# Optimization experiments

Measured on AMD Instinct MI355X. Metric: run time of the kernel, lower is better.

Reference implementation:

```python
import jax, jax.numpy as jnp
import numpy as np

N = 100000
E = 1600000
IN, HID, OUT = 128, 64, 32


def setup_inputs() -> dict:
    key = jax.random.key(0)
    k1, k2, k3, k4, k5, k6 = jax.random.split(key, 6)
    x = jax.random.normal(k1, (N, IN), dtype=jnp.float32)
    edge_index = jax.random.randint(k2, (2, E), 0, N, dtype=jnp.int64)
    # Glorot-style init for the two GCNConv layers (weight + bias each)
    W1 = jax.random.normal(k3, (IN, HID), dtype=jnp.float32) / np.sqrt(IN)
    b1 = jnp.zeros((HID,), dtype=jnp.float32)
    W2 = jax.random.normal(k4, (HID, OUT), dtype=jnp.float32) / np.sqrt(HID)
    b2 = jnp.zeros((OUT,), dtype=jnp.float32)
    return {"x": x, "edge_index": edge_index, "W1": W1, "b1": b1, "W2": W2, "b2": b2}


def _gcn_norm(edge_index, n, dtype):
    """Add self-loops and compute symmetric normalization coefficients.
    Returns (row, col, norm) where norm[e] = deg[row]^-1/2 * deg[col]^-1/2."""
    loops = jnp.tile(jnp.arange(n, dtype=edge_index.dtype)[None, :], (2, 1))
    ei = jnp.concatenate([edge_index, loops], axis=1)  # [2, E+N]
    row, col = ei[0], ei[1]
    deg = jax.ops.segment_sum(jnp.ones(col.shape, dtype), col, num_segments=n)
    dinv = jnp.where(deg > 0, jax.lax.rsqrt(deg), 0.0)
    norm = dinv[row] * dinv[col]
    return row, col, norm


def _gcn_conv(h, W, b, row, col, norm, n):
    h = h @ W                                   # [N, F_out] dense transform first
    msg = h[row] * norm[:, None]                # gather + edge-normalize
    out = jax.ops.segment_sum(msg, col, num_segments=n)  # scatter-add
    return out + b


def reference(x, edge_index, W1, b1, W2, b2):
    n = x.shape[0]
    row, col, norm = _gcn_norm(edge_index, n, x.dtype)
    h = jax.nn.relu(_gcn_conv(x, W1, b1, row, col, norm, n))
    return _gcn_conv(h, W2, b2, row, col, norm, n)
```

## Files before the change

kernel.cpp:

```cpp
#include <hip/hip_runtime.h>


#define CDIV(a, b) (((a) + (b)-1) / (b))
#define EDGE_TILE 4096
#define BUCKET_CAP 4608

__device__ inline unsigned short f2bf(float f) {
    unsigned int u = __float_as_uint(f);
    u += 0x7FFF + ((u >> 16) & 1);
    return (unsigned short)(u >> 16);
}
__device__ inline void bf2x2(unsigned int u, float& lo, float& hi) {
    lo = __uint_as_float(u << 16);
    hi = __uint_as_float(u & 0xFFFF0000u);
}

__global__ __launch_bounds__(256, 4) void k_sort_gemm1(
    const int* __restrict__ row, const int* __restrict__ col, int e,
    int* __restrict__ gcur, int* __restrict__ bucket,
    const float* __restrict__ x, const float* __restrict__ W,
    unsigned short* __restrict__ hb, int n, int nb_sort) {
    __shared__ int smem[8192];
    int t = threadIdx.x;
    if ((int)blockIdx.x < nb_sort) {
        int* lstart = smem;
        int* rbase  = smem + 512;
        int* hist   = smem + 1024;
        int* ent    = smem + 1536;
        unsigned short* bid = (unsigned short*)(smem + 5632);
        int base = blockIdx.x * EDGE_TILE;
        int cnt = min(EDGE_TILE, e - base);
        hist[t] = 0; hist[t + 256] = 0;
        __syncthreads();
        for (int i = t; i < cnt; i += 256) atomicAdd(&hist[col[base + i] >> 8], 1);
        __syncthreads();
        int h0 = hist[2 * t], h1 = hist[2 * t + 1];
        int sum2 = h0 + h1;
        rbase[t] = sum2;
        __syncthreads();
        for (int d = 1; d < 256; d <<= 1) {
            int v = (t >= d) ? rbase[t - d] : 0;
            __syncthreads();
            rbase[t] += v;
            __syncthreads();
        }
        int excl2 = rbase[t] - sum2;
        __syncthreads();
        lstart[2 * t] = excl2;
        lstart[2 * t + 1] = excl2 + h0;
        for (int b = t; b < 512; b += 256) {
            int hbv = hist[b];
            rbase[b] = (hbv > 0) ? atomicAdd(&gcur[b], hbv) : 0;
            hist[b] = 0;
        }
        __syncthreads();
        for (int i = t; i < cnt; i += 256) {
            int c = col[base + i], r = row[base + i];
            int b = c >> 8;
            int rk = atomicAdd(&hist[b], 1);
            int p = lstart[b] + rk;
            ent[p] = ((c & 255) << 17) | r;
            bid[p] = (unsigned short)b;
        }
        __syncthreads();
        for (int i = t; i < cnt; i += 256) {
            int b = bid[i];
            int gi = rbase[b] + (i - lstart[b]);
            if (gi < BUCKET_CAP) bucket[(size_t)b * BUCKET_CAP + gi] = ent[i];
        }
    } else {
        float4* xs = (float4*)smem;
        int base = ((int)blockIdx.x - nb_sort) * 64;
        int nodes = min(64, n - base);
        const float4* xg = (const float4*)(x + (size_t)base * 128);
        int lim = nodes * 32;
#pragma unroll
        for (int i = 0; i < 8; ++i) {
            int idx = t + i * 256;
            if (idx < lim) xs[idx] = xg[idx];
        }
        __syncthreads();
        int j = t & 63, g = t >> 6;
        float acc[16];
#pragma unroll
        for (int mm = 0; mm < 16; ++mm) acc[mm] = 0.f;
#pragma unroll 8
        for (int k4 = 0; k4 < 32; ++k4) {
            float w0 = W[(k4 * 4 + 0) * 64 + j];
            float w1 = W[(k4 * 4 + 1) * 64 + j];
            float w2 = W[(k4 * 4 + 2) * 64 + j];
            float w3 = W[(k4 * 4 + 3) * 64 + j];
#pragma unroll
            for (int mm = 0; mm < 16; ++mm) {
                float4 xv = xs[(mm * 4 + g) * 32 + k4];
                acc[mm] = fmaf(xv.x, w0, acc[mm]);
                acc[mm] = fmaf(xv.y, w1, acc[mm]);
                acc[mm] = fmaf(xv.z, w2, acc[mm]);
                acc[mm] = fmaf(xv.w, w3, acc[mm]);
            }
        }
#pragma unroll
        for (int mm = 0; mm < 16; ++mm) {
            int m = base + mm * 4 + g;
            if (m < n) hb[(size_t)m * 64 + j] = f2bf(acc[mm]);
        }
    }
}

__global__ __launch_bounds__(256) void k_csr(
    const int* __restrict__ gcur, const int* __restrict__ bucket,
    int* __restrict__ csr, int* __restrict__ start, int* __restrict__ cntg,
    float* __restrict__ dinv, int n) {
    __shared__ int hist[256], lstart[256], lcur[256], sc[256];
    __shared__ int csrbuf[BUCKET_CAP];
    int b = blockIdx.x, t = threadIdx.x;
    int nb = gridDim.x;
    int* gball = csrbuf;
    int v0 = (2 * t < nb) ? min(gcur[2 * t], BUCKET_CAP) : 0;
    int v1 = (2 * t + 1 < nb) ? min(gcur[2 * t + 1], BUCKET_CAP) : 0;
    int s2 = v0 + v1;
    sc[t] = s2;
    __syncthreads();
    for (int d = 1; d < 256; d <<= 1) {
        int a = (t >= d) ? sc[t - d] : 0;
        __syncthreads();
        sc[t] += a;
        __syncthreads();
    }
    int excl2 = sc[t] - s2;
    gball[2 * t] = excl2;
    gball[2 * t + 1] = excl2 + v0;
    __syncthreads();
    int gb = gball[b];
    int nodebase = b << 8;
    int nnode = min(256, n - nodebase);
    int m = min(gcur[b], BUCKET_CAP);
    const int* ent = bucket + (size_t)b * BUCKET_CAP;
    __syncthreads();
    hist[t] = 0;
    __syncthreads();
    for (int i = t; i < m; i += 256) atomicAdd(&hist[ent[i] >> 17], 1);
    __syncthreads();
    int v = hist[t];
    lstart[t] = v;
    __syncthreads();
    for (int d = 1; d < 256; d <<= 1) {
        int a = (t >= d) ? lstart[t - d] : 0;
        __syncthreads();
        lstart[t] += a;
        __syncthreads();
    }
    int excl = lstart[t] - v;
    if (t < nnode) {
        int node = nodebase + t;
        start[node] = gb + excl;
        cntg[node] = v;
        dinv[node] = rsqrtf((float)(v + 1));
    }
    __syncthreads();
    lstart[t] = excl;
    lcur[t] = 0;
    __syncthreads();
    for (int i = t; i < m; i += 256) {
        int en = ent[i];
        int local = en >> 17;
        int rk = atomicAdd(&lcur[local], 1);
        csrbuf[lstart[local] + rk] = en & 0x1FFFF;
    }
    __syncthreads();
    for (int i = t; i < m; i += 256) csr[gb + i] = csrbuf[i];
}

__global__ __launch_bounds__(256) void k_agg1(const int* __restrict__ start,
                                              const int* __restrict__ cnt,
                                              const int* __restrict__ csr,
                                              const float* __restrict__ dinv,
                                              const unsigned short* __restrict__ hbm,
                                              const float* __restrict__ b,
                                              const float* __restrict__ W2,
                                              unsigned short* __restrict__ h2b, int n) {
    __shared__ float rowbuf[4][64];
    int node = (blockIdx.x * 256 + threadIdx.x) >> 6;
    int w = threadIdx.x >> 6;
    int lane = threadIdx.x & 63;
    int q = lane >> 3;
    int f4 = lane & 7;
    const int* cs = csr + start[node];
    int d = cnt[node];
    float dc = dinv[node];
    const uint4* hb = (const uint4*)hbm;
    float a0[8], a1[8];
#pragma unroll
    for (int k = 0; k < 8; ++k) { a0[k] = 0.f; a1[k] = 0.f; }
    int j = q;
    for (; j + 8 < d; j += 16) {
        int r0 = cs[j], r1 = cs[j + 8];
        float d0 = dinv[r0], d1 = dinv[r1];
        uint4 v0 = hb[(size_t)r0 * 8 + f4];
        uint4 v1 = hb[(size_t)r1 * 8 + f4];
        float lo, hi;
        bf2x2(v0.x, lo, hi); a0[0] = fmaf(lo, d0, a0[0]); a0[1] = fmaf(hi, d0, a0[1]);
        bf2x2(v0.y, lo, hi); a0[2] = fmaf(lo, d0, a0[2]); a0[3] = fmaf(hi, d0, a0[3]);
        bf2x2(v0.z, lo, hi); a0[4] = fmaf(lo, d0, a0[4]); a0[5] = fmaf(hi, d0, a0[5]);
        bf2x2(v0.w, lo, hi); a0[6] = fmaf(lo, d0, a0[6]); a0[7] = fmaf(hi, d0, a0[7]);
        bf2x2(v1.x, lo, hi); a1[0] = fmaf(lo, d1, a1[0]); a1[1] = fmaf(hi, d1, a1[1]);
        bf2x2(v1.y, lo, hi); a1[2] = fmaf(lo, d1, a1[2]); a1[3] = fmaf(hi, d1, a1[3]);
        bf2x2(v1.z, lo, hi); a1[4] = fmaf(lo, d1, a1[4]); a1[5] = fmaf(hi, d1, a1[5]);
        bf2x2(v1.w, lo, hi); a1[6] = fmaf(lo, d1, a1[6]); a1[7] = fmaf(hi, d1, a1[7]);
    }
    if (j < d) {
        int r = cs[j];
        float d0 = dinv[r];
        uint4 v0 = hb[(size_t)r * 8 + f4];
        float lo, hi;
        bf2x2(v0.x, lo, hi); a0[0] = fmaf(lo, d0, a0[0]); a0[1] = fmaf(hi, d0, a0[1]);
        bf2x2(v0.y, lo, hi); a0[2] = fmaf(lo, d0, a0[2]); a0[3] = fmaf(hi, d0, a0[3]);
        bf2x2(v0.z, lo, hi); a0[4] = fmaf(lo, d0, a0[4]); a0[5] = fmaf(hi, d0, a0[5]);
        bf2x2(v0.w, lo, hi); a0[6] = fmaf(lo, d0, a0[6]); a0[7] = fmaf(hi, d0, a0[7]);
    }
#pragma unroll
    for (int k = 0; k < 8; ++k) a0[k] += a1[k];
#pragma unroll
    for (int k = 0; k < 8; ++k) {
        a0[k] += __shfl_xor(a0[k], 8, 64);
        a0[k] += __shfl_xor(a0[k], 16, 64);
        a0[k] += __shfl_xor(a0[k], 32, 64);
    }
    if (q == 0) {
        uint4 sv = hb[(size_t)node * 8 + f4];
        float s[8], lo, hi;
        bf2x2(sv.x, lo, hi); s[0] = lo; s[1] = hi;
        bf2x2(sv.y, lo, hi); s[2] = lo; s[3] = hi;
        bf2x2(sv.z, lo, hi); s[4] = lo; s[5] = hi;
        bf2x2(sv.w, lo, hi); s[6] = lo; s[7] = hi;
        const float4* b4 = (const float4*)b;
        float4 bv0 = b4[f4 * 2], bv1 = b4[f4 * 2 + 1];
        rowbuf[w][f4 * 8 + 0] = fmaxf(fmaf(s[0], dc, a0[0]) * dc + bv0.x, 0.f);
        rowbuf[w][f4 * 8 + 1] = fmaxf(fmaf(s[1], dc, a0[1]) * dc + bv0.y, 0.f);
        rowbuf[w][f4 * 8 + 2] = fmaxf(fmaf(s[2], dc, a0[2]) * dc + bv0.z, 0.f);
        rowbuf[w][f4 * 8 + 3] = fmaxf(fmaf(s[3], dc, a0[3]) * dc + bv0.w, 0.f);
        rowbuf[w][f4 * 8 + 4] = fmaxf(fmaf(s[4], dc, a0[4]) * dc + bv1.x, 0.f);
        rowbuf[w][f4 * 8 + 5] = fmaxf(fmaf(s[5], dc, a0[5]) * dc + bv1.y, 0.f);
        rowbuf[w][f4 * 8 + 6] = fmaxf(fmaf(s[6], dc, a0[6]) * dc + bv1.z, 0.f);
        rowbuf[w][f4 * 8 + 7] = fmaxf(fmaf(s[7], dc, a0[7]) * dc + bv1.w, 0.f);
    }
    __syncthreads();
    int jj = lane & 31, half = lane >> 5;
    const float* rw = rowbuf[w] + half * 32;
    const float* Wk = W2 + half * 32 * 32 + jj;
    float acc = 0.f;
#pragma unroll 8
    for (int k = 0; k < 32; ++k) acc = fmaf(rw[k], Wk[k * 32], acc);
    acc += __shfl_xor(acc, 32, 64);
    if (half == 0) h2b[(size_t)node * 32 + jj] = f2bf(acc * dc);
}

__global__ __launch_bounds__(256) void k_agg2(const int* __restrict__ start,
                                              const int* __restrict__ cnt,
                                              const int* __restrict__ csr,
                                              const float* __restrict__ dinv,
                                              const unsigned short* __restrict__ hbm,
                                              const float* __restrict__ b,
                                              float* __restrict__ out, int n) {
    int node = (blockIdx.x * 256 + threadIdx.x) >> 6;
    if (node >= n) return;
    int lane = threadIdx.x & 63;
    int q = lane >> 2;
    int f4 = lane & 3;
    const int* cs = csr + start[node];
    int d = cnt[node];
    const uint4* hb = (const uint4*)hbm;
    float a0[8], a1[8];
#pragma unroll
    for (int k = 0; k < 8; ++k) { a0[k] = 0.f; a1[k] = 0.f; }
    int j = q;
    for (; j + 16 < d; j += 32) {
        int r0 = cs[j], r1 = cs[j + 16];
        uint4 v0 = hb[(size_t)r0 * 4 + f4];
        uint4 v1 = hb[(size_t)r1 * 4 + f4];
        float lo, hi;
        bf2x2(v0.x, lo, hi); a0[0] += lo; a0[1] += hi;
        bf2x2(v0.y, lo, hi); a0[2] += lo; a0[3] += hi;
        bf2x2(v0.z, lo, hi); a0[4] += lo; a0[5] += hi;
        bf2x2(v0.w, lo, hi); a0[6] += lo; a0[7] += hi;
        bf2x2(v1.x, lo, hi); a1[0] += lo; a1[1] += hi;
        bf2x2(v1.y, lo, hi); a1[2] += lo; a1[3] += hi;
        bf2x2(v1.z, lo, hi); a1[4] += lo; a1[5] += hi;
        bf2x2(v1.w, lo, hi); a1[6] += lo; a1[7] += hi;
    }
    if (j < d) {
        int r = cs[j];
        uint4 v0 = hb[(size_t)r * 4 + f4];
        float lo, hi;
        bf2x2(v0.x, lo, hi); a0[0] += lo; a0[1] += hi;
        bf2x2(v0.y, lo, hi); a0[2] += lo; a0[3] += hi;
        bf2x2(v0.z, lo, hi); a0[4] += lo; a0[5] += hi;
        bf2x2(v0.w, lo, hi); a0[6] += lo; a0[7] += hi;
    }
#pragma unroll
    for (int k = 0; k < 8; ++k) a0[k] += a1[k];
#pragma unroll
    for (int k = 0; k < 8; ++k) {
        a0[k] += __shfl_xor(a0[k], 4, 64);
        a0[k] += __shfl_xor(a0[k], 8, 64);
        a0[k] += __shfl_xor(a0[k], 16, 64);
        a0[k] += __shfl_xor(a0[k], 32, 64);
    }
    if (q == 0) {
        float dc = dinv[node];
        uint4 sv = hb[(size_t)node * 4 + f4];
        float s[8], lo, hi;
        bf2x2(sv.x, lo, hi); s[0] = lo; s[1] = hi;
        bf2x2(sv.y, lo, hi); s[2] = lo; s[3] = hi;
        bf2x2(sv.z, lo, hi); s[4] = lo; s[5] = hi;
        bf2x2(sv.w, lo, hi); s[6] = lo; s[7] = hi;
        const float4* b4 = (const float4*)b;
        float4 bv0 = b4[f4 * 2], bv1 = b4[f4 * 2 + 1];
        float4 o0, o1;
        o0.x = (a0[0] + s[0]) * dc + bv0.x;
        o0.y = (a0[1] + s[1]) * dc + bv0.y;
        o0.z = (a0[2] + s[2]) * dc + bv0.z;
        o0.w = (a0[3] + s[3]) * dc + bv0.w;
        o1.x = (a0[4] + s[4]) * dc + bv1.x;
        o1.y = (a0[5] + s[5]) * dc + bv1.y;
        o1.z = (a0[6] + s[6]) * dc + bv1.z;
        o1.w = (a0[7] + s[7]) * dc + bv1.w;
        float4* o4 = (float4*)out;
        o4[(size_t)node * 8 + f4 * 2]     = o0;
        o4[(size_t)node * 8 + f4 * 2 + 1] = o1;
    }
}

extern "C" void kernel_launch(void* const* d_in, const int* in_sizes, int n_in,
                              void* d_out, int out_size, void* d_ws, size_t ws_size,
                              hipStream_t stream) {
    const float* x  = (const float*)d_in[0];
    const int*   ei = (const int*)d_in[1];
    const float* W1 = (const float*)d_in[2];
    const float* b1 = (const float*)d_in[3];
    const float* W2 = (const float*)d_in[4];
    const float* b2 = (const float*)d_in[5];
    float* out = (float*)d_out;

    const int n = in_sizes[0] / 128;
    const int e = in_sizes[1] / 2;
    const int* rowp = ei;
    const int* colp = ei + e;

    const int nbuck = CDIV(n, 256);
    const int nb_sort = CDIV(e, EDGE_TILE);
    const int nb_gemm1 = CDIV(n, 64);

    int*   gcur  = (int*)d_ws;
    int*   start = gcur + 512;
    int*   cnt   = start + n;
    float* dinv  = (float*)(cnt + n);
    int*   csr   = (int*)(dinv + n);
    unsigned short* h1b = (unsigned short*)(csr + e);
    int*   bucket = (int*)(h1b + (size_t)n * 64);
    unsigned short* h2b = (unsigned short*)bucket;

    hipMemsetAsync(gcur, 0, 512 * sizeof(int), stream);

    k_sort_gemm1<<<nb_sort + nb_gemm1, 256, 0, stream>>>(
        rowp, colp, e, gcur, bucket, x, W1, h1b, n, nb_sort);
    k_csr<<<nbuck, 256, 0, stream>>>(gcur, bucket, csr, start, cnt, dinv, n);

    k_agg1<<<CDIV(n * 64, 256), 256, 0, stream>>>(start, cnt, csr, dinv, h1b, b1, W2, h2b, n);
    k_agg2<<<CDIV(n * 64, 256), 256, 0, stream>>>(start, cnt, csr, dinv, h2b, b2, out, n);
}
```

Measured before the change: 268.0 us.

## Switch intermediates to fp16, double sort tile, drop per-edge bucket ids

Intermediate features are now stored as fp16 instead of bf16, which changes only the conversion cost and the precision, not the bytes moved. The sort phase processes 8192 edges per block instead of 4096, halving the number of sort blocks and global atomic reservations. It also stops storing a per-entry bucket id and instead finds each entry's bucket with a binary search over lstart during scatter. Shared memory grows, so the launch bound drops to 3 blocks per CU, which may reduce occupancy for the GEMM blocks.

```diff
diff --git a/kernel.cpp b/kernel.cpp
--- a/kernel.cpp
+++ b/kernel.cpp
@@ -1,75 +1,81 @@
 #include <hip/hip_runtime.h>
+#include <hip/hip_fp16.h>
 
 
 #define CDIV(a, b) (((a) + (b)-1) / (b))
-#define EDGE_TILE 4096
+#define EDGE_TILE 8192
 #define BUCKET_CAP 4608
 
-__device__ inline unsigned short f2bf(float f) {
-    unsigned int u = __float_as_uint(f);
-    u += 0x7FFF + ((u >> 16) & 1);
-    return (unsigned short)(u >> 16);
-}
-__device__ inline void bf2x2(unsigned int u, float& lo, float& hi) {
-    lo = __uint_as_float(u << 16);
-    hi = __uint_as_float(u & 0xFFFF0000u);
-}
-
-__global__ __launch_bounds__(256, 4) void k_sort_gemm1(
+__device__ inline unsigned short f2h(float f) {
+    __half h = __float2half_rn(f);
+    return __half_as_ushort(h);
+}
+__device__ inline void h2x2(unsigned int u, float& lo, float& hi) {
+    __half2 h = *reinterpret_cast<__half2*>(&u);
+    lo = __low2float(h);
+    hi = __high2float(h);
+}
+
+__global__ __launch_bounds__(256, 3) void k_sort_gemm1(
     const int* __restrict__ row, const int* __restrict__ col, int e,
     int* __restrict__ gcur, int* __restrict__ bucket,
     const float* __restrict__ x, const float* __restrict__ W,
     unsigned short* __restrict__ hb, int n, int nb_sort) {
-    __shared__ int smem[8192];
+    __shared__ float4 smem4[2560];
     int t = threadIdx.x;
     if ((int)blockIdx.x < nb_sort) {
-        int* lstart = smem;
-        int* rbase  = smem + 512;
-        int* hist   = smem + 1024;
-        int* ent    = smem + 1536;
-        unsigned short* bid = (unsigned short*)(smem + 5632);
+        int* ints   = (int*)smem4;
+        int* hist   = ints;
+        int* lstart = ints + 512;
+        int* rbase  = ints + 1024;
+        int* lcur   = ints + 1536;
+        int* ent    = ints + 2048;
         int base = blockIdx.x * EDGE_TILE;
         int cnt = min(EDGE_TILE, e - base);
+        int nbuck = (n + 255) >> 8;
         hist[t] = 0; hist[t + 256] = 0;
         __syncthreads();
         for (int i = t; i < cnt; i += 256) atomicAdd(&hist[col[base + i] >> 8], 1);
         __syncthreads();
         int h0 = hist[2 * t], h1 = hist[2 * t + 1];
         int sum2 = h0 + h1;
-        rbase[t] = sum2;
+        lcur[t] = sum2;
         __syncthreads();
         for (int d = 1; d < 256; d <<= 1) {
-            int v = (t >= d) ? rbase[t - d] : 0;
+            int v = (t >= d) ? lcur[t - d] : 0;
             __syncthreads();
-            rbase[t] += v;
+            lcur[t] += v;
             __syncthreads();
         }
-        int excl2 = rbase[t] - sum2;
-        __syncthreads();
+        int excl2 = lcur[t] - sum2;
         lstart[2 * t] = excl2;
         lstart[2 * t + 1] = excl2 + h0;
+        __syncthreads();
         for (int b = t; b < 512; b += 256) {
             int hbv = hist[b];
             rbase[b] = (hbv > 0) ? atomicAdd(&gcur[b], hbv) : 0;
-            hist[b] = 0;
+            lcur[b] = 0;
         }
         __syncthreads();
         for (int i = t; i < cnt; i += 256) {
             int c = col[base + i], r = row[base + i];
             int b = c >> 8;
-            int rk = atomicAdd(&hist[b], 1);
-            int p = lstart[b] + rk;
-            ent[p] = ((c & 255) << 17) | r;
-            bid[p] = (unsigned short)b;
+            int rk = atomicAdd(&lcur[b], 1);
+            ent[lstart[b] + rk] = ((c & 255) << 17) | r;
         }
         __syncthreads();
         for (int i = t; i < cnt; i += 256) {
-            int b = bid[i];
+            int lo = 0, hi = nbuck - 1;
+            while (lo < hi) {
+                int mid = (lo + hi + 1) >> 1;
+                if (lstart[mid] <= i) lo = mid; else hi = mid - 1;
+            }
+            int b = lo;
             int gi = rbase[b] + (i - lstart[b]);
             if (gi < BUCKET_CAP) bucket[(size_t)b * BUCKET_CAP + gi] = ent[i];
         }
     } else {
-        float4* xs = (float4*)smem;
+        float4* xs = smem4;
         int base = ((int)blockIdx.x - nb_sort) * 64;
         int nodes = min(64, n - base);
         const float4* xg = (const float4*)(x + (size_t)base * 128);
@@ -102,7 +108,7 @@
 #pragma unroll
         for (int mm = 0; mm < 16; ++mm) {
             int m = base + mm * 4 + g;
-            if (m < n) hb[(size_t)m * 64 + j] = f2bf(acc[mm]);
+            if (m < n) hb[(size_t)m * 64 + j] = f2h(acc[mm]);
         }
     }
 }
@@ -199,24 +205,24 @@
         uint4 v0 = hb[(size_t)r0 * 8 + f4];
         uint4 v1 = hb[(size_t)r1 * 8 + f4];
         float lo, hi;
-        bf2x2(v0.x, lo, hi); a0[0] = fmaf(lo, d0, a0[0]); a0[1] = fmaf(hi, d0, a0[1]);
-        bf2x2(v0.y, lo, hi); a0[2] = fmaf(lo, d0, a0[2]); a0[3] = fmaf(hi, d0, a0[3]);
-        bf2x2(v0.z, lo, hi); a0[4] = fmaf(lo, d0, a0[4]); a0[5] = fmaf(hi, d0, a0[5]);
-        bf2x2(v0.w, lo, hi); a0[6] = fmaf(lo, d0, a0[6]); a0[7] = fmaf(hi, d0, a0[7]);
-        bf2x2(v1.x, lo, hi); a1[0] = fmaf(lo, d1, a1[0]); a1[1] = fmaf(hi, d1, a1[1]);
-        bf2x2(v1.y, lo, hi); a1[2] = fmaf(lo, d1, a1[2]); a1[3] = fmaf(hi, d1, a1[3]);
-        bf2x2(v1.z, lo, hi); a1[4] = fmaf(lo, d1, a1[4]); a1[5] = fmaf(hi, d1, a1[5]);
-        bf2x2(v1.w, lo, hi); a1[6] = fmaf(lo, d1, a1[6]); a1[7] = fmaf(hi, d1, a1[7]);
+        h2x2(v0.x, lo, hi); a0[0] = fmaf(lo, d0, a0[0]); a0[1] = fmaf(hi, d0, a0[1]);
+        h2x2(v0.y, lo, hi); a0[2] = fmaf(lo, d0, a0[2]); a0[3] = fmaf(hi, d0, a0[3]);
+        h2x2(v0.z, lo, hi); a0[4] = fmaf(lo, d0, a0[4]); a0[5] = fmaf(hi, d0, a0[5]);
+        h2x2(v0.w, lo, hi); a0[6] = fmaf(lo, d0, a0[6]); a0[7] = fmaf(hi, d0, a0[7]);
+        h2x2(v1.x, lo, hi); a1[0] = fmaf(lo, d1, a1[0]); a1[1] = fmaf(hi, d1, a1[1]);
+        h2x2(v1.y, lo, hi); a1[2] = fmaf(lo, d1, a1[2]); a1[3] = fmaf(hi, d1, a1[3]);
+        h2x2(v1.z, lo, hi); a1[4] = fmaf(lo, d1, a1[4]); a1[5] = fmaf(hi, d1, a1[5]);
+        h2x2(v1.w, lo, hi); a1[6] = fmaf(lo, d1, a1[6]); a1[7] = fmaf(hi, d1, a1[7]);
     }
     if (j < d) {
         int r = cs[j];
         float d0 = dinv[r];
         uint4 v0 = hb[(size_t)r * 8 + f4];
         float lo, hi;
-        bf2x2(v0.x, lo, hi); a0[0] = fmaf(lo, d0, a0[0]); a0[1] = fmaf(hi, d0, a0[1]);
-        bf2x2(v0.y, lo, hi); a0[2] = fmaf(lo, d0, a0[2]); a0[3] = fmaf(hi, d0, a0[3]);
-        bf2x2(v0.z, lo, hi); a0[4] = fmaf(lo, d0, a0[4]); a0[5] = fmaf(hi, d0, a0[5]);
-        bf2x2(v0.w, lo, hi); a0[6] = fmaf(lo, d0, a0[6]); a0[7] = fmaf(hi, d0, a0[7]);
+        h2x2(v0.x, lo, hi); a0[0] = fmaf(lo, d0, a0[0]); a0[1] = fmaf(hi, d0, a0[1]);
+        h2x2(v0.y, lo, hi); a0[2] = fmaf(lo, d0, a0[2]); a0[3] = fmaf(hi, d0, a0[3]);
+        h2x2(v0.z, lo, hi); a0[4] = fmaf(lo, d0, a0[4]); a0[5] = fmaf(hi, d0, a0[5]);
+        h2x2(v0.w, lo, hi); a0[6] = fmaf(lo, d0, a0[6]); a0[7] = fmaf(hi, d0, a0[7]);
     }
 #pragma unroll
     for (int k = 0; k < 8; ++k) a0[k] += a1[k];
@@ -229,10 +235,10 @@
     if (q == 0) {
         uint4 sv = hb[(size_t)node * 8 + f4];
         float s[8], lo, hi;
-        bf2x2(sv.x, lo, hi); s[0] = lo; s[1] = hi;
-        bf2x2(sv.y, lo, hi); s[2] = lo; s[3] = hi;
-        bf2x2(sv.z, lo, hi); s[4] = lo; s[5] = hi;
-        bf2x2(sv.w, lo, hi); s[6] = lo; s[7] = hi;
+        h2x2(sv.x, lo, hi); s[0] = lo; s[1] = hi;
+        h2x2(sv.y, lo, hi); s[2] = lo; s[3] = hi;
+        h2x2(sv.z, lo, hi); s[4] = lo; s[5] = hi;
+        h2x2(sv.w, lo, hi); s[6] = lo; s[7] = hi;
         const float4* b4 = (const float4*)b;
         float4 bv0 = b4[f4 * 2], bv1 = b4[f4 * 2 + 1];
         rowbuf[w][f4 * 8 + 0] = fmaxf(fmaf(s[0], dc, a0[0]) * dc + bv0.x, 0.f);
@@ -252,7 +258,7 @@
 #pragma unroll 8
     for (int k = 0; k < 32; ++k) acc = fmaf(rw[k], Wk[k * 32], acc);
     acc += __shfl_xor(acc, 32, 64);
-    if (half == 0) h2b[(size_t)node * 32 + jj] = f2bf(acc * dc);
+    if (half == 0) h2b[(size_t)node * 32 + jj] = f2h(acc * dc);
 }
 
 __global__ __launch_bounds__(256) void k_agg2(const int* __restrict__ start,
@@ -279,23 +285,23 @@
         uint4 v0 = hb[(size_t)r0 * 4 + f4];
         uint4 v1 = hb[(size_t)r1 * 4 + f4];
         float lo, hi;
-        bf2x2(v0.x, lo, hi); a0[0] += lo; a0[1] += hi;
-        bf2x2(v0.y, lo, hi); a0[2] += lo; a0[3] += hi;
-        bf2x2(v0.z, lo, hi); a0[4] += lo; a0[5] += hi;
-        bf2x2(v0.w, lo, hi); a0[6] += lo; a0[7] += hi;
-        bf2x2(v1.x, lo, hi); a1[0] += lo; a1[1] += hi;
-        bf2x2(v1.y, lo, hi); a1[2] += lo; a1[3] += hi;
-        bf2x2(v1.z, lo, hi); a1[4] += lo; a1[5] += hi;
-        bf2x2(v1.w, lo, hi); a1[6] += lo; a1[7] += hi;
+        h2x2(v0.x, lo, hi); a0[0] += lo; a0[1] += hi;
+        h2x2(v0.y, lo, hi); a0[2] += lo; a0[3] += hi;
+        h2x2(v0.z, lo, hi); a0[4] += lo; a0[5] += hi;
+        h2x2(v0.w, lo, hi); a0[6] += lo; a0[7] += hi;
+        h2x2(v1.x, lo, hi); a1[0] += lo; a1[1] += hi;
+        h2x2(v1.y, lo, hi); a1[2] += lo; a1[3] += hi;
+        h2x2(v1.z, lo, hi); a1[4] += lo; a1[5] += hi;
+        h2x2(v1.w, lo, hi); a1[6] += lo; a1[7] += hi;
     }
     if (j < d) {
         int r = cs[j];
         uint4 v0 = hb[(size_t)r * 4 + f4];
         float lo, hi;
-        bf2x2(v0.x, lo, hi); a0[0] += lo; a0[1] += hi;
-        bf2x2(v0.y, lo, hi); a0[2] += lo; a0[3] += hi;
-        bf2x2(v0.z, lo, hi); a0[4] += lo; a0[5] += hi;
-        bf2x2(v0.w, lo, hi); a0[6] += lo; a0[7] += hi;
+        h2x2(v0.x, lo, hi); a0[0] += lo; a0[1] += hi;
+        h2x2(v0.y, lo, hi); a0[2] += lo; a0[3] += hi;
+        h2x2(v0.z, lo, hi); a0[4] += lo; a0[5] += hi;
+        h2x2(v0.w, lo, hi); a0[6] += lo; a0[7] += hi;
     }
 #pragma unroll
     for (int k = 0; k < 8; ++k) a0[k] += a1[k];
@@ -310,10 +316,10 @@
         float dc = dinv[node];
         uint4 sv = hb[(size_t)node * 4 + f4];
         float s[8], lo, hi;
-        bf2x2(sv.x, lo, hi); s[0] = lo; s[1] = hi;
-        bf2x2(sv.y, lo, hi); s[2] = lo; s[3] = hi;
-        bf2x2(sv.z, lo, hi); s[4] = lo; s[5] = hi;
-        bf2x2(sv.w, lo, hi); s[6] = lo; s[7] = hi;
+        h2x2(sv.x, lo, hi); s[0] = lo; s[1] = hi;
+        h2x2(sv.y, lo, hi); s[2] = lo; s[3] = hi;
+        h2x2(sv.z, lo, hi); s[4] = lo; s[5] = hi;
+        h2x2(sv.w, lo, hi); s[6] = lo; s[7] = hi;
         const float4* b4 = (const float4*)b;
         float4 bv0 = b4[f4 * 2], bv1 = b4[f4 * 2 + 1];
         float4 o0, o1;
@@ -356,16 +362,16 @@
     int*   cnt   = start + n;
     float* dinv  = (float*)(cnt + n);
     int*   csr   = (int*)(dinv + n);
-    unsigned short* h1b = (unsigned short*)(csr + e);
-    int*   bucket = (int*)(h1b + (size_t)n * 64);
-    unsigned short* h2b = (unsigned short*)bucket;
+    unsigned short* h1h = (unsigned short*)(csr + e);
+    int*   bucket = (int*)(h1h + (size_t)n * 64);
+    unsigned short* h2h = (unsigned short*)bucket;
 
     hipMemsetAsync(gcur, 0, 512 * sizeof(int), stream);
 
     k_sort_gemm1<<<nb_sort + nb_gemm1, 256, 0, stream>>>(
-        rowp, colp, e, gcur, bucket, x, W1, h1b, n, nb_sort);
+        rowp, colp, e, gcur, bucket, x, W1, h1h, n, nb_sort);
     k_csr<<<nbuck, 256, 0, stream>>>(gcur, bucket, csr, start, cnt, dinv, n);
 
-    k_agg1<<<CDIV(n * 64, 256), 256, 0, stream>>>(start, cnt, csr, dinv, h1b, b1, W2, h2b, n);
-    k_agg2<<<CDIV(n * 64, 256), 256, 0, stream>>>(start, cnt, csr, dinv, h2b, b2, out, n);
-}
+    k_agg1<<<CDIV(n * 64, 256), 256, 0, stream>>>(start, cnt, csr, dinv, h1h, b1, W2, h2h, n);
+    k_agg2<<<CDIV(n * 64, 256), 256, 0, stream>>>(start, cnt, csr, dinv, h2h, b2, out, n);
+}
```

Result: faster. 258.6 us (-3.5%).
